# Optimization experiments

Hardware: AMD Instinct MI355X
Metric: run time of the kernel (lower is better)

The kernel has to match this reference:

```python
import jax, jax.numpy as jnp
from jax import lax
import numpy as np


def setup_inputs() -> dict:
    key = jax.random.key(0)
    ks = jax.random.split(key, 9)
    B, T, F, E, H, O = 64, 512, 64, 256, 512, 128
    s = lambda k, shape, fan: jax.random.normal(k, shape, jnp.float32) / np.sqrt(fan)
    return {
        "x": jax.random.normal(ks[0], (B, T, F), jnp.float32),
        "W_emb": s(ks[1], (E, F), F),
        "b_emb": jnp.zeros((E,), jnp.float32),
        "W_ih": s(ks[2], (4 * H, E), E),
        "W_hh": s(ks[3], (4 * H, H), H),
        "b_ih": jnp.zeros((4 * H,), jnp.float32),
        "b_hh": jnp.zeros((4 * H,), jnp.float32),
        "W_fc": s(ks[4], (O, H), H),
        "b_fc": jnp.zeros((O,), jnp.float32),
    }


def reference(x, W_emb, b_emb, W_ih, W_hh, b_ih, b_hh, W_fc, b_fc):
    # Linear embedding: [B,T,F] -> [B,T,E]
    e = jnp.einsum("btf,ef->bte", x, W_emb) + b_emb
    # Precompute input-side gate projections once (big GEMM): [B,T,4H]
    xg = jnp.einsum("bte,ge->btg", e, W_ih) + b_ih + b_hh
    B = x.shape[0]
    H = W_hh.shape[1]
    W_hh_T = W_hh.T  # [H,4H]

    def step(carry, xt):
        h, c = carry
        gates = xt + h @ W_hh_T  # [B,4H]
        i, f, g, o = jnp.split(gates, 4, axis=-1)  # PyTorch LSTM gate order
        i = jax.nn.sigmoid(i)
        f = jax.nn.sigmoid(f)
        g = jnp.tanh(g)
        o = jax.nn.sigmoid(o)
        c = f * c + i * g
        h = o * jnp.tanh(c)
        return (h, c), h

    h0 = jnp.zeros((B, H), x.dtype)
    _, hs = lax.scan(step, (h0, h0), jnp.swapaxes(xg, 0, 1))  # hs: [T,B,H]
    # AdaptiveAvgPool1d(1) over time -> mean over T
    pooled = hs.mean(axis=0)  # [B,H]
    return pooled @ W_fc.T + b_fc  # [B,O]
```

## Files before the change

kernel.cpp:

```cpp
#include <hip/hip_runtime.h>
#include <math.h>

#define TS 512
#define NB 64
#define NF 64
#define NE 256
#define NH 512
#define NO 128

#define NGRP 4
#define NSLC 32
#define RPG  16

#define OFF_WCOMB 0
#define OFF_BCOMB 131072
#define OFF_HBUF  133120
#define OFF_POOL  198656

typedef short bf16x8 __attribute__((ext_vector_type(8)));
typedef float f32x4 __attribute__((ext_vector_type(4)));
typedef unsigned long long u64;
typedef unsigned int u32;

union F8 { bf16x8 s; unsigned short u[8]; };

__device__ __forceinline__ unsigned short f2bf(float f) {
    unsigned u = __float_as_uint(f);
    u += 0x7fffu + ((u >> 16) & 1u);
    return (unsigned short)(u >> 16);
}
__device__ __forceinline__ float bf2f(unsigned short h) {
    return __uint_as_float(((unsigned)h) << 16);
}
__device__ __forceinline__ float fast_sigmoid(float v) {
    return 1.f / (1.f + __expf(-v));
}
__device__ __forceinline__ float fast_tanh(float v) {
    return 1.f - 2.f / (1.f + __expf(2.f * v));
}
__device__ __forceinline__ u32 aload(const u32* p) {
    return __hip_atomic_load(p, __ATOMIC_RELAXED, __HIP_MEMORY_SCOPE_AGENT);
}

__global__ __launch_bounds__(256) void k_wcomb(const float* __restrict__ W_emb,
                                               const float* __restrict__ b_emb,
                                               const float* __restrict__ W_ih,
                                               const float* __restrict__ b_ih,
                                               const float* __restrict__ b_hh,
                                               float* __restrict__ W_comb,
                                               float* __restrict__ b_comb) {
    __shared__ float wih[4][NE];
    int g0 = blockIdx.x * 4;
    for (int i = threadIdx.x; i < 4 * NE; i += 256)
        wih[i >> 8][i & 255] = W_ih[(size_t)g0 * NE + i];
    __syncthreads();
    int gl = threadIdx.x >> 6, f = threadIdx.x & 63;
    float acc = 0.f;
    for (int e = 0; e < NE; ++e) acc += wih[gl][e] * W_emb[e * NF + f];
    W_comb[(size_t)(g0 + gl) * NF + f] = acc;
    if (f == 0) {
        float a2 = 0.f;
        for (int e = 0; e < NE; ++e) a2 += wih[gl][e] * b_emb[e];
        b_comb[g0 + gl] = a2 + b_ih[g0 + gl] + b_hh[g0 + gl];
    }
}

__global__ __launch_bounds__(512, 1) void k_lstm(const float* __restrict__ x,
                                                 const float* __restrict__ W_hh,
                                                 const float* __restrict__ W_comb,
                                                 const float* __restrict__ b_comb,
                                                 u32* __restrict__ hbuf,
                                                 float* __restrict__ pooled) {
    const int wg = blockIdx.x;
    const int grp = wg & 3;
    const int slc = wg >> 2;
    const int tid = threadIdx.x;
    const int lane = tid & 63, wave = tid >> 6;
    const int m4 = lane & 15;
    const int qq = lane >> 4;

    const int mtn = (wave < 6) ? 2 : 3;
    int kts[3];
    kts[0] = (wave < 6) ? 2 * wave : 12 + 2 * (wave - 6);
    kts[1] = kts[0] + 1;
    kts[2] = (wave < 6) ? 0 : 16 + (wave - 6);

    __shared__ __align__(16) float part[8 * 64 * 20];
    __shared__ float bcl[64];

    F8 bhi[4][3], blo[4][3];
    #pragma unroll
    for (int nt = 0; nt < 4; ++nt) {
        const int grow = nt * NH + slc * 16 + m4;
        #pragma unroll
        for (int k = 0; k < 3; ++k) {
            if (k < mtn) {
                const int kt = kts[k];
                const float* wp = (kt < 16)
                    ? W_hh   + (size_t)grow * NH + kt * 32 + qq * 8
                    : W_comb + (size_t)grow * NF + (kt - 16) * 32 + qq * 8;
                const float4 w0 = *(const float4*)wp;
                const float4 w1 = *(const float4*)(wp + 4);
                float wf[8] = {w0.x, w0.y, w0.z, w0.w, w1.x, w1.y, w1.z, w1.w};
                #pragma unroll
                for (int e = 0; e < 8; ++e) {
                    unsigned short hb = f2bf(wf[e]);
                    bhi[nt][k].u[e] = hb;
                    blo[nt][k].u[e] = f2bf(wf[e] - bf2f(hb));
                }
            }
        }
    }

    if (tid < 64) bcl[tid] = b_comb[(tid >> 4) * NH + slc * 16 + (tid & 15)];

    F8 ahi[3], alo[3];
    #pragma unroll
    for (int k = 0; k < 3; ++k) {
        ahi[k].s = (bf16x8){0, 0, 0, 0, 0, 0, 0, 0};
        alo[k].s = (bf16x8){0, 0, 0, 0, 0, 0, 0, 0};
    }
    float4 xpa = make_float4(0.f, 0.f, 0.f, 0.f), xpb = xpa;
    if (wave >= 6) {
        const int xoff = (wave - 6) * 32 + qq * 8;
        const float* xr0 = x + ((size_t)(grp * RPG + m4) * TS + 0) * NF + xoff;
        const float4 a = ((const float4*)xr0)[0];
        const float4 b4 = ((const float4*)xr0)[1];
        float xf[8] = {a.x, a.y, a.z, a.w, b4.x, b4.y, b4.z, b4.w};
        #pragma unroll
        for (int e = 0; e < 8; ++e) {
            unsigned short hb = f2bf(xf[e]);
            ahi[2].u[e] = hb;
            alo[2].u[e] = f2bf(xf[e] - bf2f(hb));
        }
        const float* xr1 = x + ((size_t)(grp * RPG + m4) * TS + 1) * NF + xoff;
        xpa = ((const float4*)xr1)[0];
        xpb = ((const float4*)xr1)[1];
    }

    float c_reg = 0.f, hsum = 0.f;
    __syncthreads();

    for (int t = 0; t < TS; ++t) {
        const bool last = (t + 1 == TS);
        const int p = t & 1;

        f32x4 acc[4][3];
        #pragma unroll
        for (int nt = 0; nt < 4; ++nt)
            #pragma unroll
            for (int c = 0; c < 3; ++c) acc[nt][c] = (f32x4){0.f, 0.f, 0.f, 0.f};
        #pragma unroll
        for (int k = 0; k < 3; ++k) {
            if (k < mtn) {
                const bf16x8 ah = ahi[k].s;
                const bf16x8 al = alo[k].s;
                #pragma unroll
                for (int nt = 0; nt < 4; ++nt) {
                    acc[nt][0] = __builtin_amdgcn_mfma_f32_16x16x32_bf16(ah, bhi[nt][k].s, acc[nt][0], 0, 0, 0);
                    acc[nt][1] = __builtin_amdgcn_mfma_f32_16x16x32_bf16(al, bhi[nt][k].s, acc[nt][1], 0, 0, 0);
                    acc[nt][2] = __builtin_amdgcn_mfma_f32_16x16x32_bf16(ah, blo[nt][k].s, acc[nt][2], 0, 0, 0);
                }
            }
        }
        #pragma unroll
        for (int nt = 0; nt < 4; ++nt) {
            const f32x4 a = acc[nt][0] + acc[nt][1] + acc[nt][2];
            *(float4*)&part[wave * 1280 + (nt * 16 + m4) * 20 + qq * 4] =
                make_float4(a.x, a.y, a.z, a.w);
        }
        __syncthreads();

        const unsigned tg2 = (unsigned)(((t + 1) & 3) ^ 2);
        u32* const slab = hbuf + ((size_t)(p * NGRP + grp)) * 8192;

        if (tid < 256) {
            const int j = tid >> 4, b = tid & 15;
            float v[4];
            #pragma unroll
            for (int ty = 0; ty < 4; ++ty) {
                const int n_loc = ty * 16 + j;
                float s = bcl[n_loc];
                #pragma unroll
                for (int w = 0; w < 8; ++w) s += part[w * 1280 + n_loc * 20 + b];
                v[ty] = s;
            }
            const float iv = fast_sigmoid(v[0]);
            const float fv = fast_sigmoid(v[1]);
            const float gv = fast_tanh(v[2]);
            const float ov = fast_sigmoid(v[3]);
            c_reg = fv * c_reg + iv * gv;
            const float h = ov * fast_tanh(c_reg);
            hsum += h;
            if (!last) {
                const unsigned short hb = f2bf(h);
                const unsigned short lb = f2bf(h - bf2f(hb));
                const u32 pk = ((u32)hb << 16) | ((u32)lb & 0xFFFCu) | tg2;
                __hip_atomic_store(&slab[slc * 256 + tid], pk,
                                   __ATOMIC_RELAXED, __HIP_MEMORY_SCOPE_AGENT);
            }
        }
        __syncthreads();

        if (!last) {
            const u32* b0 = slab + (kts[0] * 4 + qq) * 128 + m4;
            const u32* b1 = slab + (kts[1] * 4 + qq) * 128 + m4;
            u32 wd[16];
            #pragma unroll
            for (int j = 0; j < 8; ++j) wd[j] = aload(b0 + j * 16);
            #pragma unroll
            for (int j = 0; j < 8; ++j) wd[8 + j] = aload(b1 + j * 16);
            int guard = 0;
            for (;;) {
                u32 bad = 0;
                #pragma unroll
                for (int i = 0; i < 16; ++i) bad |= (wd[i] & 3) ^ tg2;
                if (bad == 0) break;
                if (guard < 8)       __builtin_amdgcn_s_sleep(1);
                else if (guard < 64) __builtin_amdgcn_s_sleep(4);
                else                 __builtin_amdgcn_s_sleep(16);
                #pragma unroll
                for (int j = 0; j < 8; ++j) wd[j] = aload(b0 + j * 16);
                #pragma unroll
                for (int j = 0; j < 8; ++j) wd[8 + j] = aload(b1 + j * 16);
                if (++guard > (1 << 20)) break;
            }
            #pragma unroll
            for (int j = 0; j < 8; ++j) {
                ahi[0].u[j] = (unsigned short)(wd[j] >> 16);
                alo[0].u[j] = (unsigned short)(wd[j] & 0xFFFCu);
                ahi[1].u[j] = (unsigned short)(wd[8 + j] >> 16);
                alo[1].u[j] = (unsigned short)(wd[8 + j] & 0xFFFCu);
            }
            if (wave >= 6) {
                const int xoff = (wave - 6) * 32 + qq * 8;
                float xf[8] = {xpa.x, xpa.y, xpa.z, xpa.w, xpb.x, xpb.y, xpb.z, xpb.w};
                #pragma unroll
                for (int e = 0; e < 8; ++e) {
                    unsigned short hb = f2bf(xf[e]);
                    ahi[2].u[e] = hb;
                    alo[2].u[e] = f2bf(xf[e] - bf2f(hb));
                }
                if (t + 2 < TS) {
                    const float* xr = x + ((size_t)(grp * RPG + m4) * TS + (t + 2)) * NF + xoff;
                    xpa = ((const float4*)xr)[0];
                    xpb = ((const float4*)xr)[1];
                }
            }
        }
    }

    if (tid < 256) {
        const int j = tid >> 4, b = tid & 15;
        pooled[(size_t)(grp * RPG + b) * NH + slc * 16 + j] = hsum * (1.f / TS);
    }
}

__global__ __launch_bounds__(256) void k_fc(const float* __restrict__ pooled,
                                            const float* __restrict__ W_fc,
                                            const float* __restrict__ b_fc,
                                            float* __restrict__ out) {
    __shared__ float pl[2][NH];
    const int b0 = blockIdx.x * 2;
    for (int i = threadIdx.x; i < 2 * NH; i += 256)
        pl[i >> 9][i & 511] = pooled[(size_t)b0 * NH + i];
    __syncthreads();
    const int o = threadIdx.x & 127, bl = threadIdx.x >> 7;
    const float* wr = W_fc + (size_t)o * NH;
    float acc = 0.f;
    #pragma unroll 4
    for (int k = 0; k < NH; k += 4) {
        const float4 wv = *(const float4*)&wr[k];
        acc += pl[bl][k] * wv.x + pl[bl][k + 1] * wv.y +
               pl[bl][k + 2] * wv.z + pl[bl][k + 3] * wv.w;
    }
    out[(size_t)(b0 + bl) * NO + o] = acc + b_fc[o];
}

extern "C" void kernel_launch(void* const* d_in, const int* in_sizes, int n_in,
                              void* d_out, int out_size, void* d_ws, size_t ws_size,
                              hipStream_t stream) {
    const float* x     = (const float*)d_in[0];
    const float* W_emb = (const float*)d_in[1];
    const float* b_emb = (const float*)d_in[2];
    const float* W_ih  = (const float*)d_in[3];
    const float* W_hh  = (const float*)d_in[4];
    const float* b_ih  = (const float*)d_in[5];
    const float* b_hh  = (const float*)d_in[6];
    const float* W_fc  = (const float*)d_in[7];
    const float* b_fc  = (const float*)d_in[8];
    float* out = (float*)d_out;
    float* ws  = (float*)d_ws;

    float* W_comb = ws + OFF_WCOMB;
    float* b_comb = ws + OFF_BCOMB;
    u32*   hbuf   = (u32*)(ws + OFF_HBUF);
    float* pooled = ws + OFF_POOL;

    hipLaunchKernelGGL(k_wcomb, dim3(512), dim3(256), 0, stream,
                       W_emb, b_emb, W_ih, b_ih, b_hh, W_comb, b_comb);
    hipLaunchKernelGGL(k_lstm,  dim3(128), dim3(512), 0, stream,
                       x, W_hh, W_comb, b_comb, hbuf, pooled);
    hipLaunchKernelGGL(k_fc,    dim3(32),  dim3(256), 0, stream,
                       pooled, W_fc, b_fc, out);
}
```

Before: 1.408 ms.

## Halve LSTM workgroups, give each 32 hidden units and all 512 threads

The persistent LSTM kernel drops from 128 to 64 workgroups, so each covers 32 hidden units (128 gate rows) instead of 16. All 8 waves now split the recurrent K dimension evenly, and the input projection is spread across wave pairs. All 512 threads compute cell updates and publish h, which halves the number of producers each consumer must poll per step. The cost is twice the register-held weights per wave (more VGPR pressure), an extra LDS reduction round with an added barrier, and single accumulators that chain MFMAs serially.

```diff
diff --git a/kernel.cpp b/kernel.cpp
--- a/kernel.cpp
+++ b/kernel.cpp
@@ -9,7 +9,7 @@
 #define NO 128
 
 #define NGRP 4
-#define NSLC 32
+#define NSLC 16
 #define RPG  16
 
 #define OFF_WCOMB 0
@@ -78,51 +78,61 @@
     const int lane = tid & 63, wave = tid >> 6;
     const int m4 = lane & 15;
     const int qq = lane >> 4;
-
-    const int mtn = (wave < 6) ? 2 : 3;
-    int kts[3];
-    kts[0] = (wave < 6) ? 2 * wave : 12 + 2 * (wave - 6);
-    kts[1] = kts[0] + 1;
-    kts[2] = (wave < 6) ? 0 : 16 + (wave - 6);
+    const int kt0 = 2 * wave;
+    const int xoff = (wave & 1) * 32 + qq * 8;
+    const int ch = tid >> 4, bb = tid & 15;
 
     __shared__ __align__(16) float part[8 * 64 * 20];
-    __shared__ float bcl[64];
-
-    F8 bhi[4][3], blo[4][3];
+
+    F8 bhi[8][2], blo[8][2];
     #pragma unroll
-    for (int nt = 0; nt < 4; ++nt) {
-        const int grow = nt * NH + slc * 16 + m4;
-        #pragma unroll
-        for (int k = 0; k < 3; ++k) {
-            if (k < mtn) {
-                const int kt = kts[k];
-                const float* wp = (kt < 16)
-                    ? W_hh   + (size_t)grow * NH + kt * 32 + qq * 8
-                    : W_comb + (size_t)grow * NF + (kt - 16) * 32 + qq * 8;
-                const float4 w0 = *(const float4*)wp;
-                const float4 w1 = *(const float4*)(wp + 4);
-                float wf[8] = {w0.x, w0.y, w0.z, w0.w, w1.x, w1.y, w1.z, w1.w};
-                #pragma unroll
-                for (int e = 0; e < 8; ++e) {
-                    unsigned short hb = f2bf(wf[e]);
-                    bhi[nt][k].u[e] = hb;
-                    blo[nt][k].u[e] = f2bf(wf[e] - bf2f(hb));
-                }
-            }
-        }
-    }
-
-    if (tid < 64) bcl[tid] = b_comb[(tid >> 4) * NH + slc * 16 + (tid & 15)];
-
-    F8 ahi[3], alo[3];
+    for (int nt = 0; nt < 8; ++nt) {
+        const int n_loc = nt * 16 + m4;
+        const int grow = (n_loc >> 5) * NH + slc * 32 + (n_loc & 31);
+        #pragma unroll
+        for (int k = 0; k < 2; ++k) {
+            const float* wp = W_hh + (size_t)grow * NH + (kt0 + k) * 32 + qq * 8;
+            const float4 w0 = *(const float4*)wp;
+            const float4 w1 = *(const float4*)(wp + 4);
+            float wf[8] = {w0.x, w0.y, w0.z, w0.w, w1.x, w1.y, w1.z, w1.w};
+            #pragma unroll
+            for (int e = 0; e < 8; ++e) {
+                unsigned short hb = f2bf(wf[e]);
+                bhi[nt][k].u[e] = hb;
+                blo[nt][k].u[e] = f2bf(wf[e] - bf2f(hb));
+            }
+        }
+    }
+    F8 bxhi[2], bxlo[2];
     #pragma unroll
-    for (int k = 0; k < 3; ++k) {
+    for (int i = 0; i < 2; ++i) {
+        const int nt = (wave >> 1) * 2 + i;
+        const int n_loc = nt * 16 + m4;
+        const int grow = (n_loc >> 5) * NH + slc * 32 + (n_loc & 31);
+        const float* wp = W_comb + (size_t)grow * NF + xoff;
+        const float4 w0 = *(const float4*)wp;
+        const float4 w1 = *(const float4*)(wp + 4);
+        float wf[8] = {w0.x, w0.y, w0.z, w0.w, w1.x, w1.y, w1.z, w1.w};
+        #pragma unroll
+        for (int e = 0; e < 8; ++e) {
+            unsigned short hb = f2bf(wf[e]);
+            bxhi[i].u[e] = hb;
+            bxlo[i].u[e] = f2bf(wf[e] - bf2f(hb));
+        }
+    }
+
+    const float bc0 = b_comb[0 * NH + slc * 32 + ch];
+    const float bc1 = b_comb[1 * NH + slc * 32 + ch];
+    const float bc2 = b_comb[2 * NH + slc * 32 + ch];
+    const float bc3 = b_comb[3 * NH + slc * 32 + ch];
+
+    F8 ahi[2], alo[2], axh, axl;
+    #pragma unroll
+    for (int k = 0; k < 2; ++k) {
         ahi[k].s = (bf16x8){0, 0, 0, 0, 0, 0, 0, 0};
         alo[k].s = (bf16x8){0, 0, 0, 0, 0, 0, 0, 0};
     }
-    float4 xpa = make_float4(0.f, 0.f, 0.f, 0.f), xpb = xpa;
-    if (wave >= 6) {
-        const int xoff = (wave - 6) * 32 + qq * 8;
+    {
         const float* xr0 = x + ((size_t)(grp * RPG + m4) * TS + 0) * NF + xoff;
         const float4 a = ((const float4*)xr0)[0];
         const float4 b4 = ((const float4*)xr0)[1];
@@ -130,81 +140,87 @@
         #pragma unroll
         for (int e = 0; e < 8; ++e) {
             unsigned short hb = f2bf(xf[e]);
-            ahi[2].u[e] = hb;
-            alo[2].u[e] = f2bf(xf[e] - bf2f(hb));
-        }
+            axh.u[e] = hb;
+            axl.u[e] = f2bf(xf[e] - bf2f(hb));
+        }
+    }
+    float4 xpa, xpb;
+    {
         const float* xr1 = x + ((size_t)(grp * RPG + m4) * TS + 1) * NF + xoff;
         xpa = ((const float4*)xr1)[0];
         xpb = ((const float4*)xr1)[1];
     }
 
     float c_reg = 0.f, hsum = 0.f;
-    __syncthreads();
 
     for (int t = 0; t < TS; ++t) {
         const bool last = (t + 1 == TS);
         const int p = t & 1;
 
-        f32x4 acc[4][3];
+        f32x4 acc[8];
+        #pragma unroll
+        for (int nt = 0; nt < 8; ++nt) acc[nt] = (f32x4){0.f, 0.f, 0.f, 0.f};
+        #pragma unroll
+        for (int nt = 0; nt < 8; ++nt) {
+            #pragma unroll
+            for (int k = 0; k < 2; ++k) {
+                acc[nt] = __builtin_amdgcn_mfma_f32_16x16x32_bf16(ahi[k].s, bhi[nt][k].s, acc[nt], 0, 0, 0);
+                acc[nt] = __builtin_amdgcn_mfma_f32_16x16x32_bf16(alo[k].s, bhi[nt][k].s, acc[nt], 0, 0, 0);
+                acc[nt] = __builtin_amdgcn_mfma_f32_16x16x32_bf16(ahi[k].s, blo[nt][k].s, acc[nt], 0, 0, 0);
+            }
+            if ((nt >> 1) == (wave >> 1)) {
+                const int i = nt & 1;
+                acc[nt] = __builtin_amdgcn_mfma_f32_16x16x32_bf16(axh.s, bxhi[i].s, acc[nt], 0, 0, 0);
+                acc[nt] = __builtin_amdgcn_mfma_f32_16x16x32_bf16(axl.s, bxhi[i].s, acc[nt], 0, 0, 0);
+                acc[nt] = __builtin_amdgcn_mfma_f32_16x16x32_bf16(axh.s, bxlo[i].s, acc[nt], 0, 0, 0);
+            }
+        }
+
         #pragma unroll
         for (int nt = 0; nt < 4; ++nt)
-            #pragma unroll
-            for (int c = 0; c < 3; ++c) acc[nt][c] = (f32x4){0.f, 0.f, 0.f, 0.f};
-        #pragma unroll
-        for (int k = 0; k < 3; ++k) {
-            if (k < mtn) {
-                const bf16x8 ah = ahi[k].s;
-                const bf16x8 al = alo[k].s;
-                #pragma unroll
-                for (int nt = 0; nt < 4; ++nt) {
-                    acc[nt][0] = __builtin_amdgcn_mfma_f32_16x16x32_bf16(ah, bhi[nt][k].s, acc[nt][0], 0, 0, 0);
-                    acc[nt][1] = __builtin_amdgcn_mfma_f32_16x16x32_bf16(al, bhi[nt][k].s, acc[nt][1], 0, 0, 0);
-                    acc[nt][2] = __builtin_amdgcn_mfma_f32_16x16x32_bf16(ah, blo[nt][k].s, acc[nt][2], 0, 0, 0);
-                }
-            }
-        }
-        #pragma unroll
-        for (int nt = 0; nt < 4; ++nt) {
-            const f32x4 a = acc[nt][0] + acc[nt][1] + acc[nt][2];
-            *(float4*)&part[wave * 1280 + (nt * 16 + m4) * 20 + qq * 4] =
-                make_float4(a.x, a.y, a.z, a.w);
-        }
+            *(f32x4*)&part[wave * 1280 + (nt * 16 + m4) * 20 + qq * 4] = acc[nt];
         __syncthreads();
+
+        float v0 = bc0, v1 = bc1;
+        #pragma unroll
+        for (int w = 0; w < 8; ++w) v0 += part[w * 1280 + ch * 20 + bb];
+        #pragma unroll
+        for (int w = 0; w < 8; ++w) v1 += part[w * 1280 + (32 + ch) * 20 + bb];
+        __syncthreads();
+
+        #pragma unroll
+        for (int nt = 4; nt < 8; ++nt)
+            *(f32x4*)&part[wave * 1280 + ((nt - 4) * 16 + m4) * 20 + qq * 4] = acc[nt];
+        __syncthreads();
+
+        float v2 = bc2, v3 = bc3;
+        #pragma unroll
+        for (int w = 0; w < 8; ++w) v2 += part[w * 1280 + ch * 20 + bb];
+        #pragma unroll
+        for (int w = 0; w < 8; ++w) v3 += part[w * 1280 + (32 + ch) * 20 + bb];
 
         const unsigned tg2 = (unsigned)(((t + 1) & 3) ^ 2);
         u32* const slab = hbuf + ((size_t)(p * NGRP + grp)) * 8192;
 
-        if (tid < 256) {
-            const int j = tid >> 4, b = tid & 15;
-            float v[4];
-            #pragma unroll
-            for (int ty = 0; ty < 4; ++ty) {
-                const int n_loc = ty * 16 + j;
-                float s = bcl[n_loc];
-                #pragma unroll
-                for (int w = 0; w < 8; ++w) s += part[w * 1280 + n_loc * 20 + b];
-                v[ty] = s;
-            }
-            const float iv = fast_sigmoid(v[0]);
-            const float fv = fast_sigmoid(v[1]);
-            const float gv = fast_tanh(v[2]);
-            const float ov = fast_sigmoid(v[3]);
-            c_reg = fv * c_reg + iv * gv;
-            const float h = ov * fast_tanh(c_reg);
-            hsum += h;
-            if (!last) {
-                const unsigned short hb = f2bf(h);
-                const unsigned short lb = f2bf(h - bf2f(hb));
-                const u32 pk = ((u32)hb << 16) | ((u32)lb & 0xFFFCu) | tg2;
-                __hip_atomic_store(&slab[slc * 256 + tid], pk,
-                                   __ATOMIC_RELAXED, __HIP_MEMORY_SCOPE_AGENT);
-            }
+        const float iv = fast_sigmoid(v0);
+        const float fv = fast_sigmoid(v1);
+        const float gv = fast_tanh(v2);
+        const float ov = fast_sigmoid(v3);
+        c_reg = fv * c_reg + iv * gv;
+        const float h = ov * fast_tanh(c_reg);
+        hsum += h;
+        if (!last) {
+            const unsigned short hb = f2bf(h);
+            const unsigned short lb = f2bf(h - bf2f(hb));
+            const u32 pk = ((u32)hb << 16) | ((u32)lb & 0xFFFCu) | tg2;
+            __hip_atomic_store(&slab[slc * 512 + tid], pk,
+                               __ATOMIC_RELAXED, __HIP_MEMORY_SCOPE_AGENT);
         }
         __syncthreads();
 
         if (!last) {
-            const u32* b0 = slab + (kts[0] * 4 + qq) * 128 + m4;
-            const u32* b1 = slab + (kts[1] * 4 + qq) * 128 + m4;
+            const u32* b0 = slab + kt0 * 512 + qq * 128 + m4;
+            const u32* b1 = b0 + 512;
             u32 wd[16];
             #pragma unroll
             for (int j = 0; j < 8; ++j) wd[j] = aload(b0 + j * 16);
@@ -232,14 +248,13 @@
                 ahi[1].u[j] = (unsigned short)(wd[8 + j] >> 16);
                 alo[1].u[j] = (unsigned short)(wd[8 + j] & 0xFFFCu);
             }
-            if (wave >= 6) {
-                const int xoff = (wave - 6) * 32 + qq * 8;
+            {
                 float xf[8] = {xpa.x, xpa.y, xpa.z, xpa.w, xpb.x, xpb.y, xpb.z, xpb.w};
                 #pragma unroll
                 for (int e = 0; e < 8; ++e) {
                     unsigned short hb = f2bf(xf[e]);
-                    ahi[2].u[e] = hb;
-                    alo[2].u[e] = f2bf(xf[e] - bf2f(hb));
+                    axh.u[e] = hb;
+                    axl.u[e] = f2bf(xf[e] - bf2f(hb));
                 }
                 if (t + 2 < TS) {
                     const float* xr = x + ((size_t)(grp * RPG + m4) * TS + (t + 2)) * NF + xoff;
@@ -250,10 +265,7 @@
         }
     }
 
-    if (tid < 256) {
-        const int j = tid >> 4, b = tid & 15;
-        pooled[(size_t)(grp * RPG + b) * NH + slc * 16 + j] = hsum * (1.f / TS);
-    }
+    pooled[(size_t)(grp * RPG + bb) * NH + slc * 32 + ch] = hsum * (1.f / TS);
 }
 
 __global__ __launch_bounds__(256) void k_fc(const float* __restrict__ pooled,
@@ -299,7 +311,7 @@
 
     hipLaunchKernelGGL(k_wcomb, dim3(512), dim3(256), 0, stream,
                        W_emb, b_emb, W_ih, b_ih, b_hh, W_comb, b_comb);
-    hipLaunchKernelGGL(k_lstm,  dim3(128), dim3(512), 0, stream,
+    hipLaunchKernelGGL(k_lstm,  dim3(64),  dim3(512), 0, stream,
                        x, W_hh, W_comb, b_comb, hbuf, pooled);
     hipLaunchKernelGGL(k_fc,    dim3(32),  dim3(256), 0, stream,
                        pooled, W_fc, b_fc, out);
```

Result: slower. 1.887 ms (+34.0%).

## Rebalance LSTM recurrent K-tiles evenly across waves and spread input projection

Applied to the files above, without the earlier changes.

Before, waves 0-5 each handled two W_hh K-tiles while waves 6-7 handled the last four W_hh tiles plus the input-projection tile, a 2-versus-3 imbalance. Now each of the 8 waves takes exactly two W_hh K-tiles. The input projection is split so each wave does one extra x-tile MFMA triple for a single gate tile (nt_x). The x conversion and prefetch now run before the spin-wait on the h exchange, so they overlap the wait, and the spin-wait sleep backoff is shortened. The aim is to cut the critical path of the per-step matmul. The cost is that every wave now loads x and carries extra registers.

```diff
diff --git a/kernel.cpp b/kernel.cpp
--- a/kernel.cpp
+++ b/kernel.cpp
@@ -78,51 +78,55 @@
     const int lane = tid & 63, wave = tid >> 6;
     const int m4 = lane & 15;
     const int qq = lane >> 4;
-
-    const int mtn = (wave < 6) ? 2 : 3;
-    int kts[3];
-    kts[0] = (wave < 6) ? 2 * wave : 12 + 2 * (wave - 6);
-    kts[1] = kts[0] + 1;
-    kts[2] = (wave < 6) ? 0 : 16 + (wave - 6);
+    const int kt0 = 2 * wave;
+    const int nt_x = wave & 3;
+    const int xoff = (wave >> 2) * 32 + qq * 8;
 
     __shared__ __align__(16) float part[8 * 64 * 20];
     __shared__ float bcl[64];
 
-    F8 bhi[4][3], blo[4][3];
+    F8 bhi[4][2], blo[4][2];
     #pragma unroll
     for (int nt = 0; nt < 4; ++nt) {
         const int grow = nt * NH + slc * 16 + m4;
         #pragma unroll
-        for (int k = 0; k < 3; ++k) {
-            if (k < mtn) {
-                const int kt = kts[k];
-                const float* wp = (kt < 16)
-                    ? W_hh   + (size_t)grow * NH + kt * 32 + qq * 8
-                    : W_comb + (size_t)grow * NF + (kt - 16) * 32 + qq * 8;
-                const float4 w0 = *(const float4*)wp;
-                const float4 w1 = *(const float4*)(wp + 4);
-                float wf[8] = {w0.x, w0.y, w0.z, w0.w, w1.x, w1.y, w1.z, w1.w};
-                #pragma unroll
-                for (int e = 0; e < 8; ++e) {
-                    unsigned short hb = f2bf(wf[e]);
-                    bhi[nt][k].u[e] = hb;
-                    blo[nt][k].u[e] = f2bf(wf[e] - bf2f(hb));
-                }
-            }
+        for (int k = 0; k < 2; ++k) {
+            const float* wp = W_hh + (size_t)grow * NH + (kt0 + k) * 32 + qq * 8;
+            const float4 w0 = *(const float4*)wp;
+            const float4 w1 = *(const float4*)(wp + 4);
+            float wf[8] = {w0.x, w0.y, w0.z, w0.w, w1.x, w1.y, w1.z, w1.w};
+            #pragma unroll
+            for (int e = 0; e < 8; ++e) {
+                unsigned short hb = f2bf(wf[e]);
+                bhi[nt][k].u[e] = hb;
+                blo[nt][k].u[e] = f2bf(wf[e] - bf2f(hb));
+            }
+        }
+    }
+    F8 bxhi, bxlo;
+    {
+        const int grow = nt_x * NH + slc * 16 + m4;
+        const float* wp = W_comb + (size_t)grow * NF + xoff;
+        const float4 w0 = *(const float4*)wp;
+        const float4 w1 = *(const float4*)(wp + 4);
+        float wf[8] = {w0.x, w0.y, w0.z, w0.w, w1.x, w1.y, w1.z, w1.w};
+        #pragma unroll
+        for (int e = 0; e < 8; ++e) {
+            unsigned short hb = f2bf(wf[e]);
+            bxhi.u[e] = hb;
+            bxlo.u[e] = f2bf(wf[e] - bf2f(hb));
         }
     }
 
     if (tid < 64) bcl[tid] = b_comb[(tid >> 4) * NH + slc * 16 + (tid & 15)];
 
-    F8 ahi[3], alo[3];
+    F8 ahi[2], alo[2], axh, axl;
     #pragma unroll
-    for (int k = 0; k < 3; ++k) {
+    for (int k = 0; k < 2; ++k) {
         ahi[k].s = (bf16x8){0, 0, 0, 0, 0, 0, 0, 0};
         alo[k].s = (bf16x8){0, 0, 0, 0, 0, 0, 0, 0};
     }
-    float4 xpa = make_float4(0.f, 0.f, 0.f, 0.f), xpb = xpa;
-    if (wave >= 6) {
-        const int xoff = (wave - 6) * 32 + qq * 8;
+    {
         const float* xr0 = x + ((size_t)(grp * RPG + m4) * TS + 0) * NF + xoff;
         const float4 a = ((const float4*)xr0)[0];
         const float4 b4 = ((const float4*)xr0)[1];
@@ -130,9 +134,12 @@
         #pragma unroll
         for (int e = 0; e < 8; ++e) {
             unsigned short hb = f2bf(xf[e]);
-            ahi[2].u[e] = hb;
-            alo[2].u[e] = f2bf(xf[e] - bf2f(hb));
-        }
+            axh.u[e] = hb;
+            axl.u[e] = f2bf(xf[e] - bf2f(hb));
+        }
+    }
+    float4 xpa, xpb;
+    {
         const float* xr1 = x + ((size_t)(grp * RPG + m4) * TS + 1) * NF + xoff;
         xpa = ((const float4*)xr1)[0];
         xpb = ((const float4*)xr1)[1];
@@ -151,16 +158,22 @@
             #pragma unroll
             for (int c = 0; c < 3; ++c) acc[nt][c] = (f32x4){0.f, 0.f, 0.f, 0.f};
         #pragma unroll
-        for (int k = 0; k < 3; ++k) {
-            if (k < mtn) {
-                const bf16x8 ah = ahi[k].s;
-                const bf16x8 al = alo[k].s;
-                #pragma unroll
-                for (int nt = 0; nt < 4; ++nt) {
-                    acc[nt][0] = __builtin_amdgcn_mfma_f32_16x16x32_bf16(ah, bhi[nt][k].s, acc[nt][0], 0, 0, 0);
-                    acc[nt][1] = __builtin_amdgcn_mfma_f32_16x16x32_bf16(al, bhi[nt][k].s, acc[nt][1], 0, 0, 0);
-                    acc[nt][2] = __builtin_amdgcn_mfma_f32_16x16x32_bf16(ah, blo[nt][k].s, acc[nt][2], 0, 0, 0);
-                }
+        for (int k = 0; k < 2; ++k) {
+            const bf16x8 ah = ahi[k].s;
+            const bf16x8 al = alo[k].s;
+            #pragma unroll
+            for (int nt = 0; nt < 4; ++nt) {
+                acc[nt][0] = __builtin_amdgcn_mfma_f32_16x16x32_bf16(ah, bhi[nt][k].s, acc[nt][0], 0, 0, 0);
+                acc[nt][1] = __builtin_amdgcn_mfma_f32_16x16x32_bf16(al, bhi[nt][k].s, acc[nt][1], 0, 0, 0);
+                acc[nt][2] = __builtin_amdgcn_mfma_f32_16x16x32_bf16(ah, blo[nt][k].s, acc[nt][2], 0, 0, 0);
+            }
+        }
+        #pragma unroll
+        for (int nt = 0; nt < 4; ++nt) {
+            if (nt == nt_x) {
+                acc[nt][0] = __builtin_amdgcn_mfma_f32_16x16x32_bf16(axh.s, bxhi.s, acc[nt][0], 0, 0, 0);
+                acc[nt][1] = __builtin_amdgcn_mfma_f32_16x16x32_bf16(axl.s, bxhi.s, acc[nt][1], 0, 0, 0);
+                acc[nt][2] = __builtin_amdgcn_mfma_f32_16x16x32_bf16(axh.s, bxlo.s, acc[nt][2], 0, 0, 0);
             }
         }
         #pragma unroll
@@ -203,49 +216,48 @@
         __syncthreads();
 
         if (!last) {
-            const u32* b0 = slab + (kts[0] * 4 + qq) * 128 + m4;
-            const u32* b1 = slab + (kts[1] * 4 + qq) * 128 + m4;
-            u32 wd[16];
-            #pragma unroll
-            for (int j = 0; j < 8; ++j) wd[j] = aload(b0 + j * 16);
-            #pragma unroll
-            for (int j = 0; j < 8; ++j) wd[8 + j] = aload(b1 + j * 16);
-            int guard = 0;
-            for (;;) {
-                u32 bad = 0;
-                #pragma unroll
-                for (int i = 0; i < 16; ++i) bad |= (wd[i] & 3) ^ tg2;
-                if (bad == 0) break;
-                if (guard < 8)       __builtin_amdgcn_s_sleep(1);
-                else if (guard < 64) __builtin_amdgcn_s_sleep(4);
-                else                 __builtin_amdgcn_s_sleep(16);
-                #pragma unroll
-                for (int j = 0; j < 8; ++j) wd[j] = aload(b0 + j * 16);
-                #pragma unroll
-                for (int j = 0; j < 8; ++j) wd[8 + j] = aload(b1 + j * 16);
-                if (++guard > (1 << 20)) break;
-            }
-            #pragma unroll
-            for (int j = 0; j < 8; ++j) {
-                ahi[0].u[j] = (unsigned short)(wd[j] >> 16);
-                alo[0].u[j] = (unsigned short)(wd[j] & 0xFFFCu);
-                ahi[1].u[j] = (unsigned short)(wd[8 + j] >> 16);
-                alo[1].u[j] = (unsigned short)(wd[8 + j] & 0xFFFCu);
-            }
-            if (wave >= 6) {
-                const int xoff = (wave - 6) * 32 + qq * 8;
+            {
                 float xf[8] = {xpa.x, xpa.y, xpa.z, xpa.w, xpb.x, xpb.y, xpb.z, xpb.w};
                 #pragma unroll
                 for (int e = 0; e < 8; ++e) {
                     unsigned short hb = f2bf(xf[e]);
-                    ahi[2].u[e] = hb;
-                    alo[2].u[e] = f2bf(xf[e] - bf2f(hb));
+                    axh.u[e] = hb;
+                    axl.u[e] = f2bf(xf[e] - bf2f(hb));
                 }
                 if (t + 2 < TS) {
                     const float* xr = x + ((size_t)(grp * RPG + m4) * TS + (t + 2)) * NF + xoff;
                     xpa = ((const float4*)xr)[0];
                     xpb = ((const float4*)xr)[1];
                 }
+            }
+            const u32* b0 = slab + kt0 * 512 + qq * 128 + m4;
+            const u32* b1 = b0 + 512;
+            u32 wd[16];
+            #pragma unroll
+            for (int j = 0; j < 8; ++j) wd[j] = aload(b0 + j * 16);
+            #pragma unroll
+            for (int j = 0; j < 8; ++j) wd[8 + j] = aload(b1 + j * 16);
+            int guard = 0;
+            for (;;) {
+                u32 bad = 0;
+                #pragma unroll
+                for (int i = 0; i < 16; ++i) bad |= (wd[i] & 3) ^ tg2;
+                if (bad == 0) break;
+                if (guard < 8)       __builtin_amdgcn_s_sleep(1);
+                else if (guard < 64) __builtin_amdgcn_s_sleep(2);
+                else                 __builtin_amdgcn_s_sleep(8);
+                #pragma unroll
+                for (int j = 0; j < 8; ++j) wd[j] = aload(b0 + j * 16);
+                #pragma unroll
+                for (int j = 0; j < 8; ++j) wd[8 + j] = aload(b1 + j * 16);
+                if (++guard > (1 << 20)) break;
+            }
+            #pragma unroll
+            for (int j = 0; j < 8; ++j) {
+                ahi[0].u[j] = (unsigned short)(wd[j] >> 16);
+                alo[0].u[j] = (unsigned short)(wd[j] & 0xFFFCu);
+                ahi[1].u[j] = (unsigned short)(wd[8 + j] >> 16);
+                alo[1].u[j] = (unsigned short)(wd[8 + j] & 0xFFFCu);
             }
         }
     }
```

Result: slower. 1.448 ms (+2.8%).

## Place LSTM groups on matching XCCs via atomic slot claiming

Applied to the files above, without the earlier changes.

The kernel now launches 512 workgroups. Each workgroup reads its hardware XCC ID and atomically claims a slice slot within that XCC's group, and the surplus workgroups exit. This keeps every batch group's 32 cooperating workgroups on one XCC, so the per-timestep h exchange can stay in that XCC's shared L2 instead of crossing dies. The polling path now uses buffer_inv plus plain global loads, and the stores are published twice (plain and atomic), with a fallback to the old atomic polling after 512 spins. The design assumes each of XCCs 0-3 gets at least 32 co-resident workgroups, and the non-coherent L2 path risks correctness or deadlock if the hardware scheduler places them differently.

```diff
diff --git a/kernel.cpp b/kernel.cpp
--- a/kernel.cpp
+++ b/kernel.cpp
@@ -16,6 +16,7 @@
 #define OFF_BCOMB 131072
 #define OFF_HBUF  133120
 #define OFF_POOL  198656
+#define OFF_CLAIM 231424
 
 typedef short bf16x8 __attribute__((ext_vector_type(8)));
 typedef float f32x4 __attribute__((ext_vector_type(4)));
@@ -41,6 +42,37 @@
 __device__ __forceinline__ u32 aload(const u32* p) {
     return __hip_atomic_load(p, __ATOMIC_RELAXED, __HIP_MEMORY_SCOPE_AGENT);
 }
+
+#define POLL16_INV(wd, b0, b1)                                        \
+    asm volatile(                                                     \
+        "buffer_inv\n\t"                                              \
+        "global_load_dword %0, %16, off\n\t"                          \
+        "global_load_dword %1, %16, off offset:64\n\t"                \
+        "global_load_dword %2, %16, off offset:128\n\t"               \
+        "global_load_dword %3, %16, off offset:192\n\t"               \
+        "global_load_dword %4, %16, off offset:256\n\t"               \
+        "global_load_dword %5, %16, off offset:320\n\t"               \
+        "global_load_dword %6, %16, off offset:384\n\t"               \
+        "global_load_dword %7, %16, off offset:448\n\t"               \
+        "global_load_dword %8, %17, off\n\t"                          \
+        "global_load_dword %9, %17, off offset:64\n\t"                \
+        "global_load_dword %10, %17, off offset:128\n\t"              \
+        "global_load_dword %11, %17, off offset:192\n\t"              \
+        "global_load_dword %12, %17, off offset:256\n\t"              \
+        "global_load_dword %13, %17, off offset:320\n\t"              \
+        "global_load_dword %14, %17, off offset:384\n\t"              \
+        "global_load_dword %15, %17, off offset:448\n\t"              \
+        "s_waitcnt vmcnt(0)"                                          \
+        : "=&v"(wd[0]), "=&v"(wd[1]), "=&v"(wd[2]), "=&v"(wd[3]),     \
+          "=&v"(wd[4]), "=&v"(wd[5]), "=&v"(wd[6]), "=&v"(wd[7]),     \
+          "=&v"(wd[8]), "=&v"(wd[9]), "=&v"(wd[10]), "=&v"(wd[11]),   \
+          "=&v"(wd[12]), "=&v"(wd[13]), "=&v"(wd[14]), "=&v"(wd[15])  \
+        : "v"(b0), "v"(b1)                                            \
+        : "memory")
+
+#define PUB_PLAIN(p, v)                                               \
+    asm volatile("global_store_dword %0, %1, off"                     \
+                 :: "v"(p), "v"(v) : "memory")
 
 __global__ __launch_bounds__(256) void k_wcomb(const float* __restrict__ W_emb,
                                                const float* __restrict__ b_emb,
@@ -48,7 +80,9 @@
                                                const float* __restrict__ b_ih,
                                                const float* __restrict__ b_hh,
                                                float* __restrict__ W_comb,
-                                               float* __restrict__ b_comb) {
+                                               float* __restrict__ b_comb,
+                                               u32* __restrict__ claim) {
+    if (blockIdx.x == 0 && threadIdx.x < 8) claim[threadIdx.x] = 0u;
     __shared__ float wih[4][NE];
     int g0 = blockIdx.x * 4;
     for (int i = threadIdx.x; i < 4 * NE; i += 256)
@@ -70,11 +104,25 @@
                                                  const float* __restrict__ W_comb,
                                                  const float* __restrict__ b_comb,
                                                  u32* __restrict__ hbuf,
+                                                 u32* __restrict__ claim,
                                                  float* __restrict__ pooled) {
-    const int wg = blockIdx.x;
-    const int grp = wg & 3;
-    const int slc = wg >> 2;
     const int tid = threadIdx.x;
+
+    u32 xcc;
+    asm volatile("s_getreg_b32 %0, hwreg(HW_REG_XCC_ID)" : "=s"(xcc));
+    xcc &= 0xFu;
+    __shared__ int slotS;
+    if (tid == 0) {
+        int slot = 1000;
+        if (xcc < NGRP) slot = (int)atomicAdd(&claim[xcc], 1u);
+        slotS = slot;
+    }
+    __syncthreads();
+    const int slot = slotS;
+    if (slot >= NSLC) return;
+    const int grp = (int)xcc;
+    const int slc = slot;
+
     const int lane = tid & 63, wave = tid >> 6;
     const int m4 = lane & 15;
     const int qq = lane >> 4;
@@ -139,6 +187,7 @@
     }
 
     float c_reg = 0.f, hsum = 0.f;
+    int mode = 0;
     __syncthreads();
 
     for (int t = 0; t < TS; ++t) {
@@ -196,8 +245,10 @@
                 const unsigned short hb = f2bf(h);
                 const unsigned short lb = f2bf(h - bf2f(hb));
                 const u32 pk = ((u32)hb << 16) | ((u32)lb & 0xFFFCu) | tg2;
-                __hip_atomic_store(&slab[slc * 256 + tid], pk,
-                                   __ATOMIC_RELAXED, __HIP_MEMORY_SCOPE_AGENT);
+                u32* const wp = &slab[slc * 256 + tid];
+                PUB_PLAIN(wp, pk);
+                __hip_atomic_store(wp, pk, __ATOMIC_RELAXED,
+                                   __HIP_MEMORY_SCOPE_AGENT);
             }
         }
         __syncthreads();
@@ -206,24 +257,30 @@
             const u32* b0 = slab + (kts[0] * 4 + qq) * 128 + m4;
             const u32* b1 = slab + (kts[1] * 4 + qq) * 128 + m4;
             u32 wd[16];
-            #pragma unroll
-            for (int j = 0; j < 8; ++j) wd[j] = aload(b0 + j * 16);
-            #pragma unroll
-            for (int j = 0; j < 8; ++j) wd[8 + j] = aload(b1 + j * 16);
             int guard = 0;
             for (;;) {
+                if (mode == 0) {
+                    POLL16_INV(wd, b0, b1);
+                } else {
+                    #pragma unroll
+                    for (int j = 0; j < 8; ++j) wd[j] = aload(b0 + j * 16);
+                    #pragma unroll
+                    for (int j = 0; j < 8; ++j) wd[8 + j] = aload(b1 + j * 16);
+                }
                 u32 bad = 0;
                 #pragma unroll
                 for (int i = 0; i < 16; ++i) bad |= (wd[i] & 3) ^ tg2;
                 if (bad == 0) break;
-                if (guard < 8)       __builtin_amdgcn_s_sleep(1);
-                else if (guard < 64) __builtin_amdgcn_s_sleep(4);
-                else                 __builtin_amdgcn_s_sleep(16);
-                #pragma unroll
-                for (int j = 0; j < 8; ++j) wd[j] = aload(b0 + j * 16);
-                #pragma unroll
-                for (int j = 0; j < 8; ++j) wd[8 + j] = aload(b1 + j * 16);
-                if (++guard > (1 << 20)) break;
+                ++guard;
+                if (mode == 0) {
+                    if (guard > 512) mode = 1;
+                    __builtin_amdgcn_s_sleep(1);
+                } else {
+                    if (guard < 8)       __builtin_amdgcn_s_sleep(1);
+                    else if (guard < 64) __builtin_amdgcn_s_sleep(2);
+                    else                 __builtin_amdgcn_s_sleep(8);
+                }
+                if (guard > (1 << 20)) break;
             }
             #pragma unroll
             for (int j = 0; j < 8; ++j) {
@@ -296,11 +353,12 @@
     float* b_comb = ws + OFF_BCOMB;
     u32*   hbuf   = (u32*)(ws + OFF_HBUF);
     float* pooled = ws + OFF_POOL;
+    u32*   claim  = (u32*)(ws + OFF_CLAIM);
 
     hipLaunchKernelGGL(k_wcomb, dim3(512), dim3(256), 0, stream,
-                       W_emb, b_emb, W_ih, b_ih, b_hh, W_comb, b_comb);
-    hipLaunchKernelGGL(k_lstm,  dim3(128), dim3(512), 0, stream,
-                       x, W_hh, W_comb, b_comb, hbuf, pooled);
+                       W_emb, b_emb, W_ih, b_ih, b_hh, W_comb, b_comb, claim);
+    hipLaunchKernelGGL(k_lstm,  dim3(512), dim3(512), 0, stream,
+                       x, W_hh, W_comb, b_comb, hbuf, claim, pooled);
     hipLaunchKernelGGL(k_fc,    dim3(32),  dim3(256), 0, stream,
                        pooled, W_fc, b_fc, out);
 }
```

Result: slower. 3.257 ms (+131.3%).
